# Kernel tuning notes

Hardware: AMD Instinct MI355X
Metric: run time of the kernel (lower is better)

The kernel has to match this reference:

```python
import jax, jax.numpy as jnp
import numpy as np
from jax import lax

N, T, F_IN = 2048, 32, 5      # stocks, lookback, OHLCV features
H, L, R = 64, 2, 8            # lstm hidden, lstm layers, relation types
GAT_H = 16                    # GAT3 hard-coded hidden width
EDGE_P = 0.05                 # relation-mask edge density
NEG = -1e9


def setup_inputs() -> dict:
    key = jax.random.key(0)
    ks = jax.random.split(key, 20)
    f32 = jnp.float32

    def nrm(k, shape, s=0.1):
        return jax.random.normal(k, shape, f32) * s

    inp = {}
    inp["inputs"] = jax.random.normal(ks[0], (N, T, F_IN), f32)
    inp["relation"] = jax.random.normal(ks[1], (N, N, R), f32)
    mask = jax.random.uniform(ks[2], (N, N)) < EDGE_P
    inp["rel_mask"] = jnp.where(mask, 0.0, NEG).astype(f32)
    # rel_weight: Linear(R, 1)
    inp["rel_w_W"] = nrm(ks[3], (1, R))
    inp["rel_w_b"] = jnp.zeros((1,), f32)
    # 2-layer LSTM (PyTorch layout: w_ih [4H, in], w_hh [4H, H], gate order i,f,g,o)
    inp["w_ih0"] = nrm(ks[4], (4 * H, F_IN)); inp["w_hh0"] = nrm(ks[5], (4 * H, H))
    inp["b_ih0"] = jnp.zeros((4 * H,), f32);  inp["b_hh0"] = jnp.zeros((4 * H,), f32)
    inp["w_ih1"] = nrm(ks[6], (4 * H, H));    inp["w_hh1"] = nrm(ks[7], (4 * H, H))
    inp["b_ih1"] = jnp.zeros((4 * H,), f32);  inp["b_hh1"] = jnp.zeros((4 * H,), f32)
    # GATConv1: hidden -> 16, heads=1 ; GATConv2: 16 -> hidden, heads=1 (lin has no bias in PyG)
    inp["gat1_W"]  = nrm(ks[8], (H, GAT_H));  inp["gat1_as"] = nrm(ks[9], (GAT_H,))
    inp["gat1_ad"] = nrm(ks[10], (GAT_H,));   inp["gat1_b"]  = jnp.zeros((GAT_H,), f32)
    inp["gat2_W"]  = nrm(ks[11], (GAT_H, H)); inp["gat2_as"] = nrm(ks[12], (H,))
    inp["gat2_ad"] = nrm(ks[13], (H,));       inp["gat2_b"]  = jnp.zeros((H,), f32)
    # fc: hidden -> 1
    inp["fc_W"] = nrm(ks[14], (H, 1)); inp["fc_b"] = jnp.zeros((1,), f32)
    return inp


def _lstm_layer(x, w_ih, w_hh, b_ih, b_hh):
    # x: [N, T, in] -> [N, T, H]; PyTorch LSTM equations, zero initial state.
    n = x.shape[0]
    h0 = jnp.zeros((n, w_hh.shape[1]), x.dtype)

    def step(carry, xt):
        h, c = carry
        g = xt @ w_ih.T + h @ w_hh.T + (b_ih + b_hh)   # [N, 4H]
        i, f, gg, o = jnp.split(g, 4, axis=-1)
        c = jax.nn.sigmoid(f) * c + jax.nn.sigmoid(i) * jnp.tanh(gg)
        h = jax.nn.sigmoid(o) * jnp.tanh(c)
        return (h, c), h

    _, hs = lax.scan(step, (h0, h0), jnp.swapaxes(x, 0, 1))  # scan over T
    return jnp.swapaxes(hs, 0, 1)


def _gat(h_in, adj, W, a_s, a_d, b):
    # Dense single-head GATConv over a boolean adjacency adj[src, dst].
    h = h_in @ W                                    # [N, out]
    e = jax.nn.leaky_relu((h @ a_s)[:, None] + (h @ a_d)[None, :], 0.2)  # [src, dst]
    e = jnp.where(adj, e, NEG)
    alpha = jax.nn.softmax(e, axis=0)               # softmax over sources per target
    return alpha.T @ h + b                          # aggregate into targets


def _forward(inputs, relation, rel_mask, rel_w_W, rel_w_b,
             w_ih0, w_hh0, b_ih0, b_hh0, w_ih1, w_hh1, b_ih1, b_hh1,
             gat1_W, gat1_as, gat1_ad, gat1_b,
             gat2_W, gat2_as, gat2_ad, gat2_b, fc_W, fc_b):
    x = _lstm_layer(inputs, w_ih0, w_hh0, b_ih0, b_hh0)
    x = _lstm_layer(x, w_ih1, w_hh1, b_ih1, b_hh1)
    x = x[:, -1, :]                                       # [N, H] last timestep
    rel_w = jnp.einsum('nmr,r->nm', relation, rel_w_W[0]) + rel_w_b[0]  # Linear(R,1)[...,-1]
    inner = x @ x.T                                       # [N, N] similarity
    weight = inner @ rel_w                                # [N, N]
    ws = jax.nn.softmax(rel_mask + weight, axis=1)        # masked entries underflow to 0
    adj = ws > 0                                          # == nonzero edge extraction
    idx = jnp.arange(adj.shape[0])
    adj = adj.at[idx, idx].set(True)                      # GATConv add_self_loops
    h = jax.nn.relu(_gat(x, adj, gat1_W, gat1_as, gat1_ad, gat1_b))
    out = _gat(h, adj, gat2_W, gat2_as, gat2_ad, gat2_b)
    return jax.nn.leaky_relu(out @ fc_W + fc_b, 0.2)      # [N, 1] prediction


def reference(inputs, relation, rel_mask, rel_w_W, rel_w_b,
              w_ih0, w_hh0, b_ih0, b_hh0, w_ih1, w_hh1, b_ih1, b_hh1,
              gat1_W, gat1_as, gat1_ad, gat1_b,
              gat2_W, gat2_as, gat2_ad, gat2_b, fc_W, fc_b):
    return _forward(inputs, relation, rel_mask, rel_w_W, rel_w_b,
                    w_ih0, w_hh0, b_ih0, b_hh0, w_ih1, w_hh1, b_ih1, b_hh1,
                    gat1_W, gat1_as, gat1_ad, gat1_b,
                    gat2_W, gat2_as, gat2_ad, gat2_b, fc_W, fc_b)
```

## Files before the change

### kernel.cpp

```cpp
#include <hip/hip_runtime.h>
#include <math.h>

#define NN 2048
#define TT 32
#define FIN 5
#define HH 64
#define G4 256
#define GATH 16

__device__ __forceinline__ float sigf(float x) {
    return 1.0f / (1.0f + __expf(-x));
}
__device__ __forceinline__ float tanh_fast(float x) {
    x = fminf(fmaxf(x, -15.0f), 15.0f);
    float t = __expf(2.0f * x);
    return (t - 1.0f) / (t + 1.0f);
}
__device__ __forceinline__ float dot4(float4 a, float4 b) {
    return a.x * b.x + a.y * b.y + a.z * b.z + a.w * b.w;
}

#define LNB 4
__global__ __launch_bounds__(256, 1)
void k_lstm(
    const float* __restrict__ inputs,
    const float* __restrict__ w_ih0, const float* __restrict__ w_hh0,
    const float* __restrict__ b_ih0, const float* __restrict__ b_hh0,
    const float* __restrict__ w_ih1, const float* __restrict__ w_hh1,
    const float* __restrict__ b_ih1, const float* __restrict__ b_hh1,
    float* __restrict__ x_out)
{
    __shared__ float x_lds[LNB * TT * FIN];
    __shared__ float hist[LNB][TT + 1][HH];
    __shared__ float g_lds[LNB * G4];
    __shared__ float h1_lds[LNB * HH];

    const int tid = threadIdx.x;
    const int n0 = blockIdx.x * LNB;
    const int g = tid;
    const int cnb = tid >> 6;
    const int ck = tid & 63;

    for (int idx = tid; idx < LNB * TT * FIN; idx += 256)
        x_lds[idx] = inputs[n0 * (TT * FIN) + idx];
    if (tid < LNB * HH) {
        hist[tid >> 6][0][tid & 63] = 0.0f;
        h1_lds[tid] = 0.0f;
    }

    {
        float4 w0[16];
        {
            const float4* p = (const float4*)(w_hh0 + g * HH);
            #pragma unroll
            for (int k = 0; k < 16; ++k) w0[k] = p[k];
        }
        float xw0 = w_ih0[g * FIN + 0];
        float xw1 = w_ih0[g * FIN + 1];
        float xw2 = w_ih0[g * FIN + 2];
        float xw3 = w_ih0[g * FIN + 3];
        float xw4 = w_ih0[g * FIN + 4];
        const float bias0 = b_ih0[g] + b_hh0[g];
        float cA = 0.0f;

        __syncthreads();

        for (int t = 1; t <= TT; ++t) {
            #pragma unroll
            for (int nb = 0; nb < LNB; ++nb) {
                const float4* hv = (const float4*)&hist[nb][t - 1][0];
                float s0 = 0.f, s1 = 0.f, s2 = 0.f, s3 = 0.f;
                #pragma unroll
                for (int k = 0; k < 4; ++k) {
                    s0 += dot4(w0[k],      hv[k]);
                    s1 += dot4(w0[4 + k],  hv[4 + k]);
                    s2 += dot4(w0[8 + k],  hv[8 + k]);
                    s3 += dot4(w0[12 + k], hv[12 + k]);
                }
                const float* xv = &x_lds[nb * (TT * FIN) + (t - 1) * FIN];
                float a = bias0 + xw0 * xv[0] + xw1 * xv[1] + xw2 * xv[2] +
                          xw3 * xv[3] + xw4 * xv[4];
                g_lds[nb * G4 + g] = a + (s0 + s1) + (s2 + s3);
            }
            __syncthreads();
            {
                const int base = cnb * G4 + ck;
                float gi = g_lds[base];
                float gf = g_lds[base + 64];
                float gg = g_lds[base + 128];
                float go = g_lds[base + 192];
                cA = sigf(gf) * cA + sigf(gi) * tanh_fast(gg);
                hist[cnb][t][ck] = sigf(go) * tanh_fast(cA);
            }
            __syncthreads();
        }
    }

    {
        float4 wi[16], wh[16];
        {
            const float4* pi = (const float4*)(w_ih1 + g * HH);
            const float4* ph = (const float4*)(w_hh1 + g * HH);
            #pragma unroll
            for (int k = 0; k < 16; ++k) { wi[k] = pi[k]; wh[k] = ph[k]; }
        }
        const float bias1 = b_ih1[g] + b_hh1[g];
        float cA = 0.0f;

        for (int t = 1; t <= TT; ++t) {
            #pragma unroll
            for (int nb = 0; nb < LNB; ++nb) {
                const float4* xv = (const float4*)&hist[nb][t][0];
                const float4* hv = (const float4*)&h1_lds[nb * HH];
                float s0 = 0.f, s1 = 0.f, s2 = 0.f, s3 = 0.f;
                float u0 = 0.f, u1 = 0.f, u2 = 0.f, u3 = 0.f;
                #pragma unroll
                for (int k = 0; k < 4; ++k) {
                    s0 += dot4(wi[k],      xv[k]);
                    s1 += dot4(wi[4 + k],  xv[4 + k]);
                    s2 += dot4(wi[8 + k],  xv[8 + k]);
                    s3 += dot4(wi[12 + k], xv[12 + k]);
                    u0 += dot4(wh[k],      hv[k]);
                    u1 += dot4(wh[4 + k],  hv[4 + k]);
                    u2 += dot4(wh[8 + k],  hv[8 + k]);
                    u3 += dot4(wh[12 + k], hv[12 + k]);
                }
                g_lds[nb * G4 + g] =
                    bias1 + ((s0 + s1) + (s2 + s3)) + ((u0 + u1) + (u2 + u3));
            }
            __syncthreads();
            {
                const int base = cnb * G4 + ck;
                float gi = g_lds[base];
                float gf = g_lds[base + 64];
                float gg = g_lds[base + 128];
                float go = g_lds[base + 192];
                cA = sigf(gf) * cA + sigf(gi) * tanh_fast(gg);
                float hA = sigf(go) * tanh_fast(cA);
                h1_lds[cnb * HH + ck] = hA;
                if (t == TT) x_out[(n0 + cnb) * HH + ck] = hA;
            }
            __syncthreads();
        }
    }
}

__global__ void k_rowmask(const float* __restrict__ rel_mask, int* __restrict__ row_full)
{
    const int i = blockIdx.x;
    const int tid = threadIdx.x;
    bool found = false;
    for (int j = tid; j < NN; j += 256)
        found |= (rel_mask[i * NN + j] == 0.0f);
    __shared__ int s_any;
    if (tid == 0) s_any = 0;
    __syncthreads();
    if (found) atomicOr(&s_any, 1);
    __syncthreads();
    if (tid == 0) row_full[i] = s_any ? 0 : 1;
}

__global__ __launch_bounds__(256) void k_h1(
    const float* __restrict__ x, const float* __restrict__ W,
    const float* __restrict__ a_s, const float* __restrict__ a_d,
    float* __restrict__ h1g, float* __restrict__ es1, float* __restrict__ ed1)
{
    __shared__ float Wl[HH * GATH];
    __shared__ float xl[16 * 65];
    __shared__ float h1l[16 * GATH];
    const int tid = threadIdx.x;
    const int n0 = blockIdx.x * 16;
    for (int idx = tid; idx < HH * GATH; idx += 256) Wl[idx] = W[idx];
    for (int idx = tid; idx < 16 * HH; idx += 256) {
        int ln = idx >> 6, k = idx & 63;
        xl[ln * 65 + k] = x[(n0 + ln) * HH + k];
    }
    __syncthreads();
    const int ln = tid >> 4, jj = tid & 15;
    float acc = 0.0f;
    #pragma unroll 8
    for (int k = 0; k < HH; ++k) acc += xl[ln * 65 + k] * Wl[k * GATH + jj];
    h1g[(n0 + ln) * GATH + jj] = acc;
    h1l[ln * GATH + jj] = acc;
    __syncthreads();
    if (tid < 16) {
        float e_s = 0.0f, e_d = 0.0f;
        #pragma unroll
        for (int t = 0; t < GATH; ++t) {
            float hv = h1l[tid * GATH + t];
            e_s += hv * a_s[t];
            e_d += hv * a_d[t];
        }
        es1[n0 + tid] = e_s;
        ed1[n0 + tid] = e_d;
    }
}

__global__ __launch_bounds__(256) void k_gat1(
    const float* __restrict__ rel_mask, const int* __restrict__ row_full,
    const float* __restrict__ h1g, const float* __restrict__ es1,
    const float* __restrict__ ed1, const float* __restrict__ gat1_b,
    float* __restrict__ hrel)
{
    const int tid = threadIdx.x;
    const int c = tid & 7;
    const int r = tid >> 3;
    const int j = blockIdx.x * 8 + c;
    const float edj = ed1[j];
    float l = 0.0f;
    float o[GATH];
    #pragma unroll
    for (int t = 0; t < GATH; ++t) o[t] = 0.0f;

    for (int i = r; i < NN; i += 32) {
        float rm = rel_mask[i * NN + j];
        bool adj = (rm == 0.0f) || (i == j) || (row_full[i] != 0);
        if (adj) {
            float e = es1[i] + edj;
            e = (e > 0.0f) ? e : 0.2f * e;
            float p = __expf(e);
            l += p;
            const float4* hv = (const float4*)(h1g + i * GATH);
            #pragma unroll
            for (int q = 0; q < 4; ++q) {
                float4 h4 = hv[q];
                o[4 * q + 0] += p * h4.x;
                o[4 * q + 1] += p * h4.y;
                o[4 * q + 2] += p * h4.z;
                o[4 * q + 3] += p * h4.w;
            }
        }
    }
    __shared__ float s_l[256];
    __shared__ float s_o[256 * GATH];
    s_l[c * 32 + r] = l;
    #pragma unroll
    for (int t = 0; t < GATH; ++t) s_o[(c * 32 + r) * GATH + t] = o[t];
    __syncthreads();
    for (int step = 16; step >= 1; step >>= 1) {
        if (r < step) {
            int a = c * 32 + r, b = a + step;
            s_l[a] += s_l[b];
            #pragma unroll
            for (int t = 0; t < GATH; ++t) s_o[a * GATH + t] += s_o[b * GATH + t];
        }
        __syncthreads();
    }
    if (tid < 128) {
        int cc = tid >> 4, jj = tid & 15;
        float v = s_o[(cc * 32) * GATH + jj] / s_l[cc * 32] + gat1_b[jj];
        hrel[(blockIdx.x * 8 + cc) * GATH + jj] = fmaxf(v, 0.0f);
    }
}

__global__ __launch_bounds__(256) void k_h2(
    const float* __restrict__ hrel, const float* __restrict__ W2,
    const float* __restrict__ a_s, const float* __restrict__ a_d,
    float* __restrict__ h2g, float* __restrict__ es2, float* __restrict__ ed2)
{
    __shared__ float Wl[GATH * HH];
    __shared__ float hl[4 * 17];
    __shared__ float h2l[4 * HH];
    const int tid = threadIdx.x;
    const int n0 = blockIdx.x * 4;
    for (int idx = tid; idx < GATH * HH; idx += 256) Wl[idx] = W2[idx];
    if (tid < 64) {
        int ln = tid >> 4, k = tid & 15;
        hl[ln * 17 + k] = hrel[(n0 + ln) * GATH + k];
    }
    __syncthreads();
    const int ln = tid >> 6, jj = tid & 63;
    float acc = 0.0f;
    #pragma unroll
    for (int k = 0; k < GATH; ++k) acc += hl[ln * 17 + k] * Wl[k * HH + jj];
    h2g[(n0 + ln) * HH + jj] = acc;
    h2l[ln * HH + jj] = acc;
    __syncthreads();
    if (tid < 4) {
        float e_s = 0.0f, e_d = 0.0f;
        #pragma unroll 16
        for (int t = 0; t < HH; ++t) {
            float hv = h2l[tid * HH + t];
            e_s += hv * a_s[t];
            e_d += hv * a_d[t];
        }
        es2[n0 + tid] = e_s;
        ed2[n0 + tid] = e_d;
    }
}

__global__ __launch_bounds__(256) void k_gat2(
    const float* __restrict__ rel_mask, const int* __restrict__ row_full,
    const float* __restrict__ h2g, const float* __restrict__ es2,
    const float* __restrict__ ed2, const float* __restrict__ gat2_b,
    const float* __restrict__ fc_W, const float* __restrict__ fc_b,
    float* __restrict__ out)
{
    const int tid = threadIdx.x;
    const int c = tid & 7;
    const int r = tid >> 3;
    const int j = blockIdx.x * 8 + c;
    const float edj = ed2[j];
    float l = 0.0f;
    float o[HH];
    #pragma unroll
    for (int t = 0; t < HH; ++t) o[t] = 0.0f;

    for (int i = r; i < NN; i += 32) {
        float rm = rel_mask[i * NN + j];
        bool adj = (rm == 0.0f) || (i == j) || (row_full[i] != 0);
        if (adj) {
            float e = es2[i] + edj;
            e = (e > 0.0f) ? e : 0.2f * e;
            float p = __expf(e);
            l += p;
            const float4* hv = (const float4*)(h2g + (size_t)i * HH);
            #pragma unroll
            for (int q = 0; q < 16; ++q) {
                float4 h4 = hv[q];
                o[4 * q + 0] += p * h4.x;
                o[4 * q + 1] += p * h4.y;
                o[4 * q + 2] += p * h4.z;
                o[4 * q + 3] += p * h4.w;
            }
        }
    }
    __shared__ float s_l[256];
    __shared__ float s_o[256 * HH];
    s_l[c * 32 + r] = l;
    #pragma unroll
    for (int t = 0; t < HH; ++t) s_o[(c * 32 + r) * HH + t] = o[t];
    __syncthreads();
    for (int step = 16; step >= 1; step >>= 1) {
        if (r < step) {
            int a = c * 32 + r, b = a + step;
            s_l[a] += s_l[b];
            #pragma unroll
            for (int t = 0; t < HH; ++t) s_o[a * HH + t] += s_o[b * HH + t];
        }
        __syncthreads();
    }
    __shared__ float s_out[8 * HH];
    {
        int cc = tid >> 5, jj = tid & 31;
        float linv = 1.0f / s_l[cc * 32];
        s_out[cc * HH + jj] = s_o[(cc * 32) * HH + jj] * linv + gat2_b[jj];
        s_out[cc * HH + jj + 32] = s_o[(cc * 32) * HH + jj + 32] * linv + gat2_b[jj + 32];
    }
    __syncthreads();
    if (tid < 8) {
        float acc = fc_b[0];
        #pragma unroll 16
        for (int t = 0; t < HH; ++t) acc += s_out[tid * HH + t] * fc_W[t];
        out[blockIdx.x * 8 + tid] = (acc > 0.0f) ? acc : 0.2f * acc;
    }
}

extern "C" void kernel_launch(void* const* d_in, const int* in_sizes, int n_in,
                              void* d_out, int out_size, void* d_ws, size_t ws_size,
                              hipStream_t stream)
{
    const float* inputs   = (const float*)d_in[0];
    const float* rel_mask = (const float*)d_in[2];
    const float* w_ih0 = (const float*)d_in[5];
    const float* w_hh0 = (const float*)d_in[6];
    const float* b_ih0 = (const float*)d_in[7];
    const float* b_hh0 = (const float*)d_in[8];
    const float* w_ih1 = (const float*)d_in[9];
    const float* w_hh1 = (const float*)d_in[10];
    const float* b_ih1 = (const float*)d_in[11];
    const float* b_hh1 = (const float*)d_in[12];
    const float* gat1_W  = (const float*)d_in[13];
    const float* gat1_as = (const float*)d_in[14];
    const float* gat1_ad = (const float*)d_in[15];
    const float* gat1_b  = (const float*)d_in[16];
    const float* gat2_W  = (const float*)d_in[17];
    const float* gat2_as = (const float*)d_in[18];
    const float* gat2_ad = (const float*)d_in[19];
    const float* gat2_b  = (const float*)d_in[20];
    const float* fc_W = (const float*)d_in[21];
    const float* fc_b = (const float*)d_in[22];
    float* out = (float*)d_out;

    float* ws = (float*)d_ws;
    float* x_out = ws;
    float* h1g = x_out + NN * HH;
    float* es1 = h1g + NN * GATH;
    float* ed1 = es1 + NN;
    float* hrel = ed1 + NN;
    float* h2g = hrel + NN * GATH;
    float* es2 = h2g + NN * HH;
    float* ed2 = es2 + NN;
    int* row_full = (int*)(ed2 + NN);

    k_lstm<<<NN / LNB, 256, 0, stream>>>(inputs, w_ih0, w_hh0, b_ih0, b_hh0,
                                         w_ih1, w_hh1, b_ih1, b_hh1, x_out);
    k_rowmask<<<NN, 256, 0, stream>>>(rel_mask, row_full);
    k_h1<<<NN / 16, 256, 0, stream>>>(x_out, gat1_W, gat1_as, gat1_ad, h1g, es1, ed1);
    k_gat1<<<NN / 8, 256, 0, stream>>>(rel_mask, row_full, h1g, es1, ed1, gat1_b, hrel);
    k_h2<<<NN / 4, 256, 0, stream>>>(hrel, gat2_W, gat2_as, gat2_ad, h2g, es2, ed2);
    k_gat2<<<NN / 8, 256, 0, stream>>>(rel_mask, row_full, h2g, es2, ed2, gat2_b,
                                       fc_W, fc_b, out);
}
```

Baseline: 516.2 us.

## Build sparse CSC edge lists once and gather over edges in GAT kernels

A new pass scans rel_mask once and builds per-destination edge lists with atomics. It also builds a list of rows that have no edges at all, which the original semantics treat as full rows. Both GAT aggregation kernels now iterate only over these lists instead of rescanning the dense 2048x2048 mask, and they parallelise over feature dimensions with a small shared-memory reduction. The gat2 kernel fuses the fc projection through a wavefront shuffle reduction. Separately, the LSTM handles 2 stocks per block instead of 4 to launch more blocks, leaving some threads idle in the cell update. Neighbour lists are capped at 256 entries, so denser graphs would be silently truncated, and the atomic ordering makes the summation order nondeterministic.

```diff
diff --git a/kernel.cpp b/kernel.cpp
--- a/kernel.cpp
+++ b/kernel.cpp
@@ -7,6 +7,7 @@
 #define HH 64
 #define G4 256
 #define GATH 16
+#define CAP 256
 
 __device__ __forceinline__ float sigf(float x) {
     return 1.0f / (1.0f + __expf(-x));
@@ -19,8 +20,12 @@
 __device__ __forceinline__ float dot4(float4 a, float4 b) {
     return a.x * b.x + a.y * b.y + a.z * b.z + a.w * b.w;
 }
-
-#define LNB 4
+__device__ __forceinline__ float lrelu_exp(float x) {
+    x = (x > 0.0f) ? x : 0.2f * x;
+    return __expf(x);
+}
+
+#define LNB 2
 __global__ __launch_bounds__(256, 1)
 void k_lstm(
     const float* __restrict__ inputs,
@@ -83,7 +88,7 @@
                 g_lds[nb * G4 + g] = a + (s0 + s1) + (s2 + s3);
             }
             __syncthreads();
-            {
+            if (tid < LNB * HH) {
                 const int base = cnb * G4 + ck;
                 float gi = g_lds[base];
                 float gf = g_lds[base + 64];
@@ -129,7 +134,7 @@
                     bias1 + ((s0 + s1) + (s2 + s3)) + ((u0 + u1) + (u2 + u3));
             }
             __syncthreads();
-            {
+            if (tid < LNB * HH) {
                 const int base = cnb * G4 + ck;
                 float gi = g_lds[base];
                 float gf = g_lds[base + 64];
@@ -145,19 +150,43 @@
     }
 }
 
-__global__ void k_rowmask(const float* __restrict__ rel_mask, int* __restrict__ row_full)
+__global__ void k_zero(int* __restrict__ cnt, int* __restrict__ nfull)
+{
+    int i = blockIdx.x * 256 + threadIdx.x;
+    if (i < NN) cnt[i] = 0;
+    if (i == 0) *nfull = 0;
+}
+
+__global__ __launch_bounds__(256) void k_edges(
+    const float* __restrict__ rel_mask,
+    int* __restrict__ cnt, int* __restrict__ csc,
+    int* __restrict__ row_full, int* __restrict__ full_list,
+    int* __restrict__ nfull)
 {
     const int i = blockIdx.x;
     const int tid = threadIdx.x;
-    bool found = false;
-    for (int j = tid; j < NN; j += 256)
-        found |= (rel_mask[i * NN + j] == 0.0f);
     __shared__ int s_any;
     if (tid == 0) s_any = 0;
     __syncthreads();
-    if (found) atomicOr(&s_any, 1);
-    __syncthreads();
-    if (tid == 0) row_full[i] = s_any ? 0 : 1;
+    bool mine = false;
+    for (int j = tid; j < NN; j += 256) {
+        float rm = rel_mask[i * NN + j];
+        bool edge = (rm == 0.0f);
+        mine |= edge;
+        if (edge && j != i) {
+            int slot = atomicAdd(&cnt[j], 1);
+            if (slot < CAP) csc[j * CAP + slot] = i;
+        }
+    }
+    if (mine) atomicOr(&s_any, 1);
+    __syncthreads();
+    if (tid == 0) {
+        row_full[i] = s_any ? 0 : 1;
+        if (!s_any) {
+            int k = atomicAdd(nfull, 1);
+            full_list[k] = i;
+        }
+    }
 }
 
 __global__ __launch_bounds__(256) void k_h1(
@@ -196,60 +225,52 @@
     }
 }
 
-__global__ __launch_bounds__(256) void k_gat1(
-    const float* __restrict__ rel_mask, const int* __restrict__ row_full,
+__global__ __launch_bounds__(256) void k_gat1s(
+    const int* __restrict__ cnt, const int* __restrict__ csc,
+    const int* __restrict__ row_full, const int* __restrict__ full_list,
+    const int* __restrict__ nfull,
     const float* __restrict__ h1g, const float* __restrict__ es1,
     const float* __restrict__ ed1, const float* __restrict__ gat1_b,
     float* __restrict__ hrel)
 {
     const int tid = threadIdx.x;
-    const int c = tid & 7;
-    const int r = tid >> 3;
-    const int j = blockIdx.x * 8 + c;
+    const int lc = tid >> 6;
+    const int grp = (tid >> 4) & 3;
+    const int d = tid & 15;
+    const int j = blockIdx.x * 4 + lc;
     const float edj = ed1[j];
-    float l = 0.0f;
-    float o[GATH];
-    #pragma unroll
-    for (int t = 0; t < GATH; ++t) o[t] = 0.0f;
-
-    for (int i = r; i < NN; i += 32) {
-        float rm = rel_mask[i * NN + j];
-        bool adj = (rm == 0.0f) || (i == j) || (row_full[i] != 0);
-        if (adj) {
-            float e = es1[i] + edj;
-            e = (e > 0.0f) ? e : 0.2f * e;
-            float p = __expf(e);
-            l += p;
-            const float4* hv = (const float4*)(h1g + i * GATH);
-            #pragma unroll
-            for (int q = 0; q < 4; ++q) {
-                float4 h4 = hv[q];
-                o[4 * q + 0] += p * h4.x;
-                o[4 * q + 1] += p * h4.y;
-                o[4 * q + 2] += p * h4.z;
-                o[4 * q + 3] += p * h4.w;
-            }
-        }
-    }
-    __shared__ float s_l[256];
-    __shared__ float s_o[256 * GATH];
-    s_l[c * 32 + r] = l;
-    #pragma unroll
-    for (int t = 0; t < GATH; ++t) s_o[(c * 32 + r) * GATH + t] = o[t];
-    __syncthreads();
-    for (int step = 16; step >= 1; step >>= 1) {
-        if (r < step) {
-            int a = c * 32 + r, b = a + step;
-            s_l[a] += s_l[b];
-            #pragma unroll
-            for (int t = 0; t < GATH; ++t) s_o[a * GATH + t] += s_o[b * GATH + t];
-        }
-        __syncthreads();
-    }
-    if (tid < 128) {
-        int cc = tid >> 4, jj = tid & 15;
-        float v = s_o[(cc * 32) * GATH + jj] / s_l[cc * 32] + gat1_b[jj];
-        hrel[(blockIdx.x * 8 + cc) * GATH + jj] = fmaxf(v, 0.0f);
+    float acc = 0.0f, l = 0.0f;
+
+    const int n = min(cnt[j], CAP);
+    const int* lst = csc + j * CAP;
+    for (int e = grp; e < n; e += 4) {
+        int i = lst[e];
+        float p = lrelu_exp(es1[i] + edj);
+        l += p;
+        acc += p * h1g[i * GATH + d];
+    }
+    if (grp == 0 && !row_full[j]) {
+        float p = lrelu_exp(es1[j] + edj);
+        l += p;
+        acc += p * h1g[j * GATH + d];
+    }
+    const int nf = *nfull;
+    for (int f = grp; f < nf; f += 4) {
+        int i = full_list[f];
+        float p = lrelu_exp(es1[i] + edj);
+        l += p;
+        acc += p * h1g[i * GATH + d];
+    }
+
+    __shared__ float sacc[4][4][GATH];
+    __shared__ float sl[4][4];
+    sacc[lc][grp][d] = acc;
+    if (d == 0) sl[lc][grp] = l;
+    __syncthreads();
+    if (grp == 0) {
+        float a = sacc[lc][0][d] + sacc[lc][1][d] + sacc[lc][2][d] + sacc[lc][3][d];
+        float L = sl[lc][0] + sl[lc][1] + sl[lc][2] + sl[lc][3];
+        hrel[j * GATH + d] = fmaxf(a / L + gat1_b[d], 0.0f);
     }
 }
 
@@ -289,70 +310,60 @@
     }
 }
 
-__global__ __launch_bounds__(256) void k_gat2(
-    const float* __restrict__ rel_mask, const int* __restrict__ row_full,
+__global__ __launch_bounds__(256) void k_gat2s(
+    const int* __restrict__ cnt, const int* __restrict__ csc,
+    const int* __restrict__ row_full, const int* __restrict__ full_list,
+    const int* __restrict__ nfull,
     const float* __restrict__ h2g, const float* __restrict__ es2,
     const float* __restrict__ ed2, const float* __restrict__ gat2_b,
     const float* __restrict__ fc_W, const float* __restrict__ fc_b,
     float* __restrict__ out)
 {
     const int tid = threadIdx.x;
-    const int c = tid & 7;
-    const int r = tid >> 3;
-    const int j = blockIdx.x * 8 + c;
+    const int grp = tid >> 6;
+    const int d = tid & 63;
+    const int j = blockIdx.x;
     const float edj = ed2[j];
-    float l = 0.0f;
-    float o[HH];
-    #pragma unroll
-    for (int t = 0; t < HH; ++t) o[t] = 0.0f;
-
-    for (int i = r; i < NN; i += 32) {
-        float rm = rel_mask[i * NN + j];
-        bool adj = (rm == 0.0f) || (i == j) || (row_full[i] != 0);
-        if (adj) {
-            float e = es2[i] + edj;
-            e = (e > 0.0f) ? e : 0.2f * e;
-            float p = __expf(e);
-            l += p;
-            const float4* hv = (const float4*)(h2g + (size_t)i * HH);
-            #pragma unroll
-            for (int q = 0; q < 16; ++q) {
-                float4 h4 = hv[q];
-                o[4 * q + 0] += p * h4.x;
-                o[4 * q + 1] += p * h4.y;
-                o[4 * q + 2] += p * h4.z;
-                o[4 * q + 3] += p * h4.w;
-            }
-        }
-    }
-    __shared__ float s_l[256];
-    __shared__ float s_o[256 * HH];
-    s_l[c * 32 + r] = l;
-    #pragma unroll
-    for (int t = 0; t < HH; ++t) s_o[(c * 32 + r) * HH + t] = o[t];
-    __syncthreads();
-    for (int step = 16; step >= 1; step >>= 1) {
-        if (r < step) {
-            int a = c * 32 + r, b = a + step;
-            s_l[a] += s_l[b];
-            #pragma unroll
-            for (int t = 0; t < HH; ++t) s_o[a * HH + t] += s_o[b * HH + t];
-        }
-        __syncthreads();
-    }
-    __shared__ float s_out[8 * HH];
-    {
-        int cc = tid >> 5, jj = tid & 31;
-        float linv = 1.0f / s_l[cc * 32];
-        s_out[cc * HH + jj] = s_o[(cc * 32) * HH + jj] * linv + gat2_b[jj];
-        s_out[cc * HH + jj + 32] = s_o[(cc * 32) * HH + jj + 32] * linv + gat2_b[jj + 32];
-    }
-    __syncthreads();
-    if (tid < 8) {
-        float acc = fc_b[0];
-        #pragma unroll 16
-        for (int t = 0; t < HH; ++t) acc += s_out[tid * HH + t] * fc_W[t];
-        out[blockIdx.x * 8 + tid] = (acc > 0.0f) ? acc : 0.2f * acc;
+    float acc = 0.0f, l = 0.0f;
+
+    const int n = min(cnt[j], CAP);
+    const int* lst = csc + j * CAP;
+    for (int e = grp; e < n; e += 4) {
+        int i = lst[e];
+        float p = lrelu_exp(es2[i] + edj);
+        l += p;
+        acc += p * h2g[i * HH + d];
+    }
+    if (grp == 0 && !row_full[j]) {
+        float p = lrelu_exp(es2[j] + edj);
+        l += p;
+        acc += p * h2g[j * HH + d];
+    }
+    const int nf = *nfull;
+    for (int f = grp; f < nf; f += 4) {
+        int i = full_list[f];
+        float p = lrelu_exp(es2[i] + edj);
+        l += p;
+        acc += p * h2g[i * HH + d];
+    }
+
+    __shared__ float sacc[4][HH];
+    __shared__ float sl[4];
+    sacc[grp][d] = acc;
+    if (d == 0) sl[grp] = l;
+    __syncthreads();
+    if (grp == 0) {
+        float a = sacc[0][d] + sacc[1][d] + sacc[2][d] + sacc[3][d];
+        float L = sl[0] + sl[1] + sl[2] + sl[3];
+        float v = a / L + gat2_b[d];
+        float t = v * fc_W[d];
+        #pragma unroll
+        for (int off = 32; off >= 1; off >>= 1)
+            t += __shfl_down(t, off, 64);
+        if (d == 0) {
+            float r = t + fc_b[0];
+            out[j] = (r > 0.0f) ? r : 0.2f * r;
+        }
     }
 }
 
@@ -391,14 +402,20 @@
     float* h2g = hrel + NN * GATH;
     float* es2 = h2g + NN * HH;
     float* ed2 = es2 + NN;
-    int* row_full = (int*)(ed2 + NN);
-
+    int* cnt = (int*)(ed2 + NN);
+    int* row_full = cnt + NN;
+    int* full_list = row_full + NN;
+    int* nfull = full_list + NN;
+    int* csc = nfull + 8;
+
+    k_zero<<<(NN + 255) / 256, 256, 0, stream>>>(cnt, nfull);
+    k_edges<<<NN, 256, 0, stream>>>(rel_mask, cnt, csc, row_full, full_list, nfull);
     k_lstm<<<NN / LNB, 256, 0, stream>>>(inputs, w_ih0, w_hh0, b_ih0, b_hh0,
                                          w_ih1, w_hh1, b_ih1, b_hh1, x_out);
-    k_rowmask<<<NN, 256, 0, stream>>>(rel_mask, row_full);
     k_h1<<<NN / 16, 256, 0, stream>>>(x_out, gat1_W, gat1_as, gat1_ad, h1g, es1, ed1);
-    k_gat1<<<NN / 8, 256, 0, stream>>>(rel_mask, row_full, h1g, es1, ed1, gat1_b, hrel);
+    k_gat1s<<<NN / 4, 256, 0, stream>>>(cnt, csc, row_full, full_list, nfull,
+                                        h1g, es1, ed1, gat1_b, hrel);
     k_h2<<<NN / 4, 256, 0, stream>>>(hrel, gat2_W, gat2_as, gat2_ad, h2g, es2, ed2);
-    k_gat2<<<NN / 8, 256, 0, stream>>>(rel_mask, row_full, h2g, es2, ed2, gat2_b,
-                                       fc_W, fc_b, out);
-}
+    k_gat2s<<<NN, 256, 0, stream>>>(cnt, csc, row_full, full_list, nfull,
+                                    h2g, es2, ed2, gat2_b, fc_W, fc_b, out);
+}
```

Result: faster. 489.0 us (-5.3%).
